# Kernel optimization log

Measured on AMD Instinct MI355X. Metric: run time of the kernel, lower is better.

The kernel has to match this reference:

```python
import jax, jax.numpy as jnp
import numpy as np

B = 8192
DIM_Q = 1024
DIM_U = 1024
NUM_CHARTS = 16
TOP_K = 2


def setup_inputs() -> dict:
    key = jax.random.key(0)
    k1, k2, k3 = jax.random.split(key, 3)
    q = jax.random.normal(k1, (B, DIM_Q), dtype=jnp.float32)
    weights = jax.random.uniform(k2, (B, NUM_CHARTS), dtype=jnp.float32)
    # W_stack init: -I + 0.01*randn per chart (dim_q == dim_u branch)
    W_stack = (-jnp.eye(DIM_Q, dtype=jnp.float32)[None, :, :]
               + 0.01 * jax.random.normal(k3, (NUM_CHARTS, DIM_U, DIM_Q), dtype=jnp.float32))
    return {"q": q, "weights": weights, "W_stack": W_stack}


def reference(q, weights, W_stack):
    # Top-k gated mixture of linear maps: out[b] = sum_{c in topk(weights[b])} w_norm[b,c] * W_stack[c] @ q[b]
    b = q.shape[0]
    w_vals, idx = jax.lax.top_k(weights, TOP_K)              # [B, k], sorted descending (matches torch.topk)
    w_norm = w_vals / jnp.clip(jnp.sum(w_vals, axis=1, keepdims=True), 1e-8, None)
    # scatter normalized weights back to dense [B, num_charts] gate matrix
    w_masked = jnp.zeros_like(weights).at[jnp.arange(b)[:, None], idx].set(w_norm)
    out = jnp.zeros((b, W_stack.shape[1]), dtype=q.dtype)
    for c in range(NUM_CHARTS):  # small fixed expert count
        out = out + w_masked[:, c:c + 1] * (q @ W_stack[c].T)  # [B, dim_u]
    return out
```

## Files before the change

### kernel.cpp

```cpp
#include <hip/hip_runtime.h>
#include <hip/hip_bf16.h>
#include <stdint.h>

#define NROWS 8192
#define DIMQ 1024
#define DIMU 1024
#define NCH 16

#define BM 128
#define BN 128
#define BK 64

typedef __attribute__((ext_vector_type(4))) float f32x4;
typedef __attribute__((ext_vector_type(8))) short bf16x8;

__device__ __forceinline__ short f2bf(float f) {
    union { __hip_bfloat16 h; short s; } u;
    u.h = __float2bfloat16(f);
    return u.s;
}

__global__ void cvt2_kernel(const float* __restrict__ q, const float* __restrict__ Ws,
                            short* __restrict__ qb, short* __restrict__ Wb) {
    const int nq = NROWS * DIMQ / 8;
    const int nw = NCH * DIMU * DIMQ / 8;
    int i0 = blockIdx.x * blockDim.x + threadIdx.x;
    int stride = gridDim.x * blockDim.x;
    for (int i = i0; i < nq; i += stride) {
        const f32x4* p = reinterpret_cast<const f32x4*>(q + (size_t)i * 8);
        f32x4 a = p[0], b = p[1];
        bf16x8 o;
        o[0] = f2bf(a[0]); o[1] = f2bf(a[1]); o[2] = f2bf(a[2]); o[3] = f2bf(a[3]);
        o[4] = f2bf(b[0]); o[5] = f2bf(b[1]); o[6] = f2bf(b[2]); o[7] = f2bf(b[3]);
        *reinterpret_cast<bf16x8*>(qb + (size_t)i * 8) = o;
    }
    for (int i = i0; i < nw; i += stride) {
        const f32x4* p = reinterpret_cast<const f32x4*>(Ws + (size_t)i * 8);
        f32x4 a = p[0], b = p[1];
        bf16x8 o;
        o[0] = f2bf(a[0]); o[1] = f2bf(a[1]); o[2] = f2bf(a[2]); o[3] = f2bf(a[3]);
        o[4] = f2bf(b[0]); o[5] = f2bf(b[1]); o[6] = f2bf(b[2]); o[7] = f2bf(b[3]);
        *reinterpret_cast<bf16x8*>(Wb + (size_t)i * 8) = o;
    }
}

__global__ void gate_kernel(const float* __restrict__ weights,
                            int* __restrict__ cnt,
                            int* __restrict__ rowlist,
                            float* __restrict__ wgt) {
    __shared__ int lcnt[NCH];
    __shared__ int lbase[NCH];
    const int t = threadIdx.x;
    const int b = blockIdx.x * blockDim.x + t;
    if (t < NCH) lcnt[t] = 0;
    __syncthreads();

    float w[NCH];
    const f32x4* wp = reinterpret_cast<const f32x4*>(weights + (size_t)b * NCH);
#pragma unroll
    for (int i = 0; i < 4; ++i) {
        f32x4 v = wp[i];
        w[i * 4 + 0] = v[0]; w[i * 4 + 1] = v[1];
        w[i * 4 + 2] = v[2]; w[i * 4 + 3] = v[3];
    }
    int i0 = 0; float v0 = w[0];
#pragma unroll
    for (int i = 1; i < NCH; ++i) if (w[i] > v0) { v0 = w[i]; i0 = i; }
    int i1 = (i0 == 0) ? 1 : 0; float v1 = w[i1];
#pragma unroll
    for (int i = 0; i < NCH; ++i) if (i != i0 && w[i] > v1) { v1 = w[i]; i1 = i; }
    float s = v0 + v1;
    s = (s < 1e-8f) ? 1e-8f : s;
    float n0 = v0 / s, n1 = v1 / s;

    int p0 = atomicAdd(&lcnt[i0], 1);
    int p1 = atomicAdd(&lcnt[i1], 1);
    __syncthreads();
    if (t < NCH) lbase[t] = atomicAdd(&cnt[t], lcnt[t]);
    __syncthreads();

    int o0 = lbase[i0] + p0;
    int o1 = lbase[i1] + p1;
    rowlist[(size_t)i0 * NROWS + o0] = b;  wgt[(size_t)i0 * NROWS + o0] = n0;
    rowlist[(size_t)i1 * NROWS + o1] = b;  wgt[(size_t)i1 * NROWS + o1] = n1;
}

__global__ __launch_bounds__(256, 3) void moe_gemm_bf(
    const short* __restrict__ qb, const short* __restrict__ Wb,
    const int* __restrict__ cnt, const int* __restrict__ rowlist,
    const float* __restrict__ wgt, float* __restrict__ out)
{
    const int id  = blockIdx.x;
    const int xcd = id & 7;
    const int k   = id >> 3;
    const int c   = xcd + ((k >> 9) << 3);
    const int kk  = k & 511;
    const int n0  = (kk & 7) * BN;
    const int m0  = (kk >> 3) * BM;

    const int count = cnt[c];
    if (m0 >= count) return;

    __shared__ short sA[BM * BK];
    __shared__ short sB[BN * BK];
    __shared__ int   sRow[BM];
    __shared__ float sW[BM];

    const int t = threadIdx.x;
    if (t < BM) {
        int gi = m0 + t;
        int r = 0; float wv_ = 0.f;
        if (gi < count) {
            r   = rowlist[(size_t)c * NROWS + gi];
            wv_ = wgt[(size_t)c * NROWS + gi];
        }
        sRow[t] = r; sW[t] = wv_;
    }
    __syncthreads();

    const short* aSrc[4];
    const short* bSrc[4];
#pragma unroll
    for (int i = 0; i < 4; ++i) {
        int ch = i * 256 + t;
        int r  = ch >> 3;
        int c8 = ch & 7;
        aSrc[i] = qb + (size_t)sRow[r] * DIMQ + c8 * 8;
        bSrc[i] = Wb + (size_t)c * ((size_t)DIMU * DIMQ) + (size_t)(n0 + r) * DIMQ + c8 * 8;
    }

    const int lane = t & 63;
    const int wv   = t >> 6;
    const int wm   = (wv >> 1) * 64;
    const int wn   = (wv & 1) * 64;
    const int rr   = lane & 15;
    const int g    = lane >> 4;

    f32x4 acc[4][4];
#pragma unroll
    for (int r = 0; r < 4; ++r)
#pragma unroll
        for (int cc = 0; cc < 4; ++cc)
            acc[r][cc] = (f32x4){0.f, 0.f, 0.f, 0.f};

    const int NKT = DIMQ / BK;
    for (int kt = 0; kt < NKT; ++kt) {
        __syncthreads();
#pragma unroll
        for (int i = 0; i < 4; ++i)
            __builtin_amdgcn_global_load_lds(aSrc[i] + kt * BK, &sA[(i * 256 + t) * 8], 16, 0, 0);
#pragma unroll
        for (int i = 0; i < 4; ++i)
            __builtin_amdgcn_global_load_lds(bSrc[i] + kt * BK, &sB[(i * 256 + t) * 8], 16, 0, 0);
        __syncthreads();

#pragma unroll
        for (int ks = 0; ks < 2; ++ks) {
            bf16x8 af[4], bfr[4];
#pragma unroll
            for (int r = 0; r < 4; ++r) {
                af[r]  = *reinterpret_cast<const bf16x8*>(&sA[(wm + r * 16 + rr) * BK + ks * 32 + g * 8]);
                bfr[r] = *reinterpret_cast<const bf16x8*>(&sB[(wn + r * 16 + rr) * BK + ks * 32 + g * 8]);
            }
#pragma unroll
            for (int r = 0; r < 4; ++r)
#pragma unroll
                for (int cc = 0; cc < 4; ++cc)
                    acc[r][cc] = __builtin_amdgcn_mfma_f32_16x16x32_bf16(af[r], bfr[cc], acc[r][cc], 0, 0, 0);
        }
    }

#pragma unroll
    for (int r = 0; r < 4; ++r) {
#pragma unroll
        for (int cc = 0; cc < 4; ++cc) {
#pragma unroll
            for (int j = 0; j < 4; ++j) {
                int rowInTile = wm + r * 16 + g * 4 + j;
                int gi = m0 + rowInTile;
                if (gi < count) {
                    int   orow = sRow[rowInTile];
                    float wgx  = sW[rowInTile];
                    int   col  = n0 + wn + cc * 16 + rr;
                    atomicAdd(&out[(size_t)orow * DIMU + col], acc[r][cc][j] * wgx);
                }
            }
        }
    }
}

#define BKF 32
#define LDSTRF 40
typedef __attribute__((ext_vector_type(4))) short s16x4;

__global__ __launch_bounds__(256, 2) void moe_gemm_f32(
    const float* __restrict__ q, const float* __restrict__ Wst,
    const int* __restrict__ cnt, const int* __restrict__ rowlist,
    const float* __restrict__ wgt, float* __restrict__ out)
{
    const int c  = blockIdx.z;
    const int n0 = blockIdx.x * BN;
    const int m0 = blockIdx.y * BM;
    const int count = cnt[c];
    if (m0 >= count) return;

    __shared__ short sA[BM * LDSTRF];
    __shared__ short sB[BN * LDSTRF];
    __shared__ int   sRow[BM];
    __shared__ float sW[BM];

    const int t = threadIdx.x;
    if (t < BM) {
        int gi = m0 + t;
        int r = 0; float w = 0.f;
        if (gi < count) {
            r = rowlist[(size_t)c * NROWS + gi];
            w = wgt[(size_t)c * NROWS + gi];
        }
        sRow[t] = r; sW[t] = w;
    }
    __syncthreads();

    const float* aBase[4];
    const float* bBase[4];
    int ldsOff[4];
#pragma unroll
    for (int i = 0; i < 4; ++i) {
        int f  = t + i * 256;
        int r  = f >> 3;
        int c4 = f & 7;
        aBase[i]  = q   + (size_t)sRow[r] * DIMQ + c4 * 4;
        bBase[i]  = Wst + (size_t)c * ((size_t)DIMU * DIMQ) + (size_t)(n0 + r) * DIMQ + c4 * 4;
        ldsOff[i] = r * LDSTRF + c4 * 4;
    }

    const int lane = t & 63;
    const int wv   = t >> 6;
    const int wm   = (wv >> 1) * 64;
    const int wn   = (wv & 1) * 64;
    const int rr   = lane & 15;
    const int g    = lane >> 4;

    f32x4 acc[4][4];
#pragma unroll
    for (int r = 0; r < 4; ++r)
#pragma unroll
        for (int cc = 0; cc < 4; ++cc)
            acc[r][cc] = (f32x4){0.f, 0.f, 0.f, 0.f};

    f32x4 pa[4], pb[4];
#pragma unroll
    for (int i = 0; i < 4; ++i) {
        pa[i] = *reinterpret_cast<const f32x4*>(aBase[i]);
        pb[i] = *reinterpret_cast<const f32x4*>(bBase[i]);
    }

    const int NKT = DIMQ / BKF;
    for (int kt = 0; kt < NKT; ++kt) {
        __syncthreads();
#pragma unroll
        for (int i = 0; i < 4; ++i) {
            s16x4 va, vb;
#pragma unroll
            for (int j = 0; j < 4; ++j) { va[j] = f2bf(pa[i][j]); vb[j] = f2bf(pb[i][j]); }
            *reinterpret_cast<s16x4*>(&sA[ldsOff[i]]) = va;
            *reinterpret_cast<s16x4*>(&sB[ldsOff[i]]) = vb;
        }
        __syncthreads();

        if (kt + 1 < NKT) {
            int k = (kt + 1) * BKF;
#pragma unroll
            for (int i = 0; i < 4; ++i) {
                pa[i] = *reinterpret_cast<const f32x4*>(aBase[i] + k);
                pb[i] = *reinterpret_cast<const f32x4*>(bBase[i] + k);
            }
        }

        bf16x8 af[4], bfr[4];
#pragma unroll
        for (int r = 0; r < 4; ++r) {
            af[r]  = *reinterpret_cast<const bf16x8*>(&sA[(wm + r * 16 + rr) * LDSTRF + g * 8]);
            bfr[r] = *reinterpret_cast<const bf16x8*>(&sB[(wn + r * 16 + rr) * LDSTRF + g * 8]);
        }
#pragma unroll
        for (int r = 0; r < 4; ++r)
#pragma unroll
            for (int cc = 0; cc < 4; ++cc)
                acc[r][cc] = __builtin_amdgcn_mfma_f32_16x16x32_bf16(af[r], bfr[cc], acc[r][cc], 0, 0, 0);
    }

#pragma unroll
    for (int r = 0; r < 4; ++r) {
#pragma unroll
        for (int cc = 0; cc < 4; ++cc) {
#pragma unroll
            for (int j = 0; j < 4; ++j) {
                int rowInTile = wm + r * 16 + g * 4 + j;
                int gi = m0 + rowInTile;
                if (gi < count) {
                    int   orow = sRow[rowInTile];
                    float w    = sW[rowInTile];
                    int   col  = n0 + wn + cc * 16 + rr;
                    atomicAdd(&out[(size_t)orow * DIMU + col], acc[r][cc][j] * w);
                }
            }
        }
    }
}

extern "C" void kernel_launch(void* const* d_in, const int* in_sizes, int n_in,
                              void* d_out, int out_size, void* d_ws, size_t ws_size,
                              hipStream_t stream) {
    const float* q  = (const float*)d_in[0];
    const float* w  = (const float*)d_in[1];
    const float* Ws = (const float*)d_in[2];
    float* out = (float*)d_out;

    const size_t qbf_bytes  = (size_t)NROWS * DIMQ * 2;
    const size_t wbf_bytes  = (size_t)NCH * DIMU * (size_t)DIMQ * 2;
    const size_t meta_bytes = 256 + (size_t)NCH * NROWS * (sizeof(int) + sizeof(float));
    char* ws = (char*)d_ws;

    if (ws_size >= qbf_bytes + wbf_bytes + meta_bytes) {
        short* qb      = (short*)ws;
        short* Wb      = (short*)(ws + qbf_bytes);
        int*   cnt     = (int*)(ws + qbf_bytes + wbf_bytes);
        int*   rowlist = (int*)(ws + qbf_bytes + wbf_bytes + 256);
        float* wgt     = (float*)(ws + qbf_bytes + wbf_bytes + 256 + (size_t)NCH * NROWS * sizeof(int));

        hipMemsetAsync(cnt, 0, 256, stream);
        hipMemsetAsync(d_out, 0, (size_t)out_size * sizeof(float), stream);

        cvt2_kernel<<<2048, 256, 0, stream>>>(q, Ws, qb, Wb);
        gate_kernel<<<NROWS / 256, 256, 0, stream>>>(w, cnt, rowlist, wgt);

        moe_gemm_bf<<<8192, 256, 0, stream>>>(qb, Wb, cnt, rowlist, wgt, out);
    } else {
        int*   cnt     = (int*)ws;
        int*   rowlist = (int*)(ws + 256);
        float* wgt     = (float*)(ws + 256 + (size_t)NCH * NROWS * sizeof(int));

        hipMemsetAsync(cnt, 0, 256, stream);
        hipMemsetAsync(d_out, 0, (size_t)out_size * sizeof(float), stream);

        gate_kernel<<<NROWS / 256, 256, 0, stream>>>(w, cnt, rowlist, wgt);

        dim3 grid(DIMU / BN, NROWS / BM, NCH);
        moe_gemm_f32<<<grid, 256, 0, stream>>>(q, Ws, cnt, rowlist, wgt, out);
    }
}
```

Baseline: 241.1 us.

## Restructure bf16 MoE GEMM with register prefetch, padded LDS and 512 threads

Replaces the direct global-to-LDS loads with register-staged loads that prefetch the next K tiles while the current tile is computed. The LDS rows are padded to avoid bank conflicts, and the block grows to 512 threads (8 waves, each computing 64x32). The XCD-aware block-id swizzle is dropped in favour of a plain 3D grid. It adds register pressure and extra barriers, and losing the swizzle may reduce L2 locality of W tiles per chart.

```diff
diff --git a/kernel.cpp b/kernel.cpp
--- a/kernel.cpp
+++ b/kernel.cpp
@@ -10,8 +10,10 @@
 #define BM 128
 #define BN 128
 #define BK 64
+#define LDSTR 72
 
 typedef __attribute__((ext_vector_type(4))) float f32x4;
+typedef __attribute__((ext_vector_type(4))) short s16x4;
 typedef __attribute__((ext_vector_type(8))) short bf16x8;
 
 __device__ __forceinline__ short f2bf(float f) {
@@ -85,24 +87,19 @@
     rowlist[(size_t)i1 * NROWS + o1] = b;  wgt[(size_t)i1 * NROWS + o1] = n1;
 }
 
-__global__ __launch_bounds__(256, 3) void moe_gemm_bf(
+__global__ __launch_bounds__(512, 4) void moe_gemm_bf(
     const short* __restrict__ qb, const short* __restrict__ Wb,
     const int* __restrict__ cnt, const int* __restrict__ rowlist,
     const float* __restrict__ wgt, float* __restrict__ out)
 {
-    const int id  = blockIdx.x;
-    const int xcd = id & 7;
-    const int k   = id >> 3;
-    const int c   = xcd + ((k >> 9) << 3);
-    const int kk  = k & 511;
-    const int n0  = (kk & 7) * BN;
-    const int m0  = (kk >> 3) * BM;
-
+    const int c  = blockIdx.z;
+    const int n0 = blockIdx.x * BN;
+    const int m0 = blockIdx.y * BM;
     const int count = cnt[c];
     if (m0 >= count) return;
 
-    __shared__ short sA[BM * BK];
-    __shared__ short sB[BN * BK];
+    __shared__ short sA[BM * LDSTR];
+    __shared__ short sB[BN * LDSTR];
     __shared__ int   sRow[BM];
     __shared__ float sW[BM];
 
@@ -118,62 +115,103 @@
     }
     __syncthreads();
 
-    const short* aSrc[4];
-    const short* bSrc[4];
-#pragma unroll
-    for (int i = 0; i < 4; ++i) {
-        int ch = i * 256 + t;
+    const short* aS[2];
+    const short* bS[2];
+    int ldsO[2];
+#pragma unroll
+    for (int i = 0; i < 2; ++i) {
+        int ch = i * 512 + t;
         int r  = ch >> 3;
         int c8 = ch & 7;
-        aSrc[i] = qb + (size_t)sRow[r] * DIMQ + c8 * 8;
-        bSrc[i] = Wb + (size_t)c * ((size_t)DIMU * DIMQ) + (size_t)(n0 + r) * DIMQ + c8 * 8;
+        aS[i]   = qb + (size_t)sRow[r] * DIMQ + c8 * 8;
+        bS[i]   = Wb + (size_t)c * ((size_t)DIMU * DIMQ) + (size_t)(n0 + r) * DIMQ + c8 * 8;
+        ldsO[i] = r * LDSTR + c8 * 8;
     }
 
     const int lane = t & 63;
     const int wv   = t >> 6;
-    const int wm   = (wv >> 1) * 64;
-    const int wn   = (wv & 1) * 64;
+    const int wm   = (wv >> 2) * 64;
+    const int wn   = (wv & 3) * 32;
     const int rr   = lane & 15;
     const int g    = lane >> 4;
 
-    f32x4 acc[4][4];
+    f32x4 acc[4][2];
 #pragma unroll
     for (int r = 0; r < 4; ++r)
 #pragma unroll
-        for (int cc = 0; cc < 4; ++cc)
-            acc[r][cc] = (f32x4){0.f, 0.f, 0.f, 0.f};
+        for (int n = 0; n < 2; ++n)
+            acc[r][n] = (f32x4){0.f, 0.f, 0.f, 0.f};
+
+    bf16x8 a0[2], b0[2], a1[2], b1[2];
+#pragma unroll
+    for (int i = 0; i < 2; ++i) {
+        a0[i] = *reinterpret_cast<const bf16x8*>(aS[i]);
+        b0[i] = *reinterpret_cast<const bf16x8*>(bS[i]);
+        a1[i] = *reinterpret_cast<const bf16x8*>(aS[i] + BK);
+        b1[i] = *reinterpret_cast<const bf16x8*>(bS[i] + BK);
+    }
+
+#define COMPUTE_STEP()                                                                              \
+    {                                                                                               \
+        _Pragma("unroll")                                                                           \
+        for (int ks = 0; ks < 2; ++ks) {                                                            \
+            bf16x8 af[4], bfr[2];                                                                   \
+            _Pragma("unroll")                                                                       \
+            for (int r = 0; r < 4; ++r)                                                             \
+                af[r]  = *reinterpret_cast<const bf16x8*>(&sA[(wm + r * 16 + rr) * LDSTR + ks * 32 + g * 8]); \
+            _Pragma("unroll")                                                                       \
+            for (int n = 0; n < 2; ++n)                                                             \
+                bfr[n] = *reinterpret_cast<const bf16x8*>(&sB[(wn + n * 16 + rr) * LDSTR + ks * 32 + g * 8]); \
+            _Pragma("unroll")                                                                       \
+            for (int r = 0; r < 4; ++r)                                                             \
+                _Pragma("unroll")                                                                   \
+                for (int n = 0; n < 2; ++n)                                                         \
+                    acc[r][n] = __builtin_amdgcn_mfma_f32_16x16x32_bf16(af[r], bfr[n], acc[r][n], 0, 0, 0); \
+        }                                                                                           \
+    }
 
     const int NKT = DIMQ / BK;
-    for (int kt = 0; kt < NKT; ++kt) {
-        __syncthreads();
-#pragma unroll
-        for (int i = 0; i < 4; ++i)
-            __builtin_amdgcn_global_load_lds(aSrc[i] + kt * BK, &sA[(i * 256 + t) * 8], 16, 0, 0);
-#pragma unroll
-        for (int i = 0; i < 4; ++i)
-            __builtin_amdgcn_global_load_lds(bSrc[i] + kt * BK, &sB[(i * 256 + t) * 8], 16, 0, 0);
-        __syncthreads();
-
-#pragma unroll
-        for (int ks = 0; ks < 2; ++ks) {
-            bf16x8 af[4], bfr[4];
-#pragma unroll
-            for (int r = 0; r < 4; ++r) {
-                af[r]  = *reinterpret_cast<const bf16x8*>(&sA[(wm + r * 16 + rr) * BK + ks * 32 + g * 8]);
-                bfr[r] = *reinterpret_cast<const bf16x8*>(&sB[(wn + r * 16 + rr) * BK + ks * 32 + g * 8]);
-            }
-#pragma unroll
-            for (int r = 0; r < 4; ++r)
-#pragma unroll
-                for (int cc = 0; cc < 4; ++cc)
-                    acc[r][cc] = __builtin_amdgcn_mfma_f32_16x16x32_bf16(af[r], bfr[cc], acc[r][cc], 0, 0, 0);
-        }
-    }
+    for (int kt2 = 0; kt2 < NKT; kt2 += 2) {
+        __syncthreads();
+#pragma unroll
+        for (int i = 0; i < 2; ++i) {
+            *reinterpret_cast<bf16x8*>(&sA[ldsO[i]]) = a0[i];
+            *reinterpret_cast<bf16x8*>(&sB[ldsO[i]]) = b0[i];
+        }
+        __syncthreads();
+        if (kt2 + 2 < NKT) {
+            int k = (kt2 + 2) * BK;
+#pragma unroll
+            for (int i = 0; i < 2; ++i) {
+                a0[i] = *reinterpret_cast<const bf16x8*>(aS[i] + k);
+                b0[i] = *reinterpret_cast<const bf16x8*>(bS[i] + k);
+            }
+        }
+        COMPUTE_STEP();
+
+        __syncthreads();
+#pragma unroll
+        for (int i = 0; i < 2; ++i) {
+            *reinterpret_cast<bf16x8*>(&sA[ldsO[i]]) = a1[i];
+            *reinterpret_cast<bf16x8*>(&sB[ldsO[i]]) = b1[i];
+        }
+        __syncthreads();
+        if (kt2 + 3 < NKT) {
+            int k = (kt2 + 3) * BK;
+#pragma unroll
+            for (int i = 0; i < 2; ++i) {
+                a1[i] = *reinterpret_cast<const bf16x8*>(aS[i] + k);
+                b1[i] = *reinterpret_cast<const bf16x8*>(bS[i] + k);
+            }
+        }
+        COMPUTE_STEP();
+    }
+#undef COMPUTE_STEP
 
 #pragma unroll
     for (int r = 0; r < 4; ++r) {
 #pragma unroll
-        for (int cc = 0; cc < 4; ++cc) {
+        for (int n = 0; n < 2; ++n) {
 #pragma unroll
             for (int j = 0; j < 4; ++j) {
                 int rowInTile = wm + r * 16 + g * 4 + j;
@@ -181,8 +219,8 @@
                 if (gi < count) {
                     int   orow = sRow[rowInTile];
                     float wgx  = sW[rowInTile];
-                    int   col  = n0 + wn + cc * 16 + rr;
-                    atomicAdd(&out[(size_t)orow * DIMU + col], acc[r][cc][j] * wgx);
+                    int   col  = n0 + wn + n * 16 + rr;
+                    atomicAdd(&out[(size_t)orow * DIMU + col], acc[r][n][j] * wgx);
                 }
             }
         }
@@ -191,7 +229,6 @@
 
 #define BKF 32
 #define LDSTRF 40
-typedef __attribute__((ext_vector_type(4))) short s16x4;
 
 __global__ __launch_bounds__(256, 2) void moe_gemm_f32(
     const float* __restrict__ q, const float* __restrict__ Wst,
@@ -335,7 +372,8 @@
         cvt2_kernel<<<2048, 256, 0, stream>>>(q, Ws, qb, Wb);
         gate_kernel<<<NROWS / 256, 256, 0, stream>>>(w, cnt, rowlist, wgt);
 
-        moe_gemm_bf<<<8192, 256, 0, stream>>>(qb, Wb, cnt, rowlist, wgt, out);
+        dim3 grid(DIMU / BN, NROWS / BM, NCH);
+        moe_gemm_bf<<<grid, 512, 0, stream>>>(qb, Wb, cnt, rowlist, wgt, out);
     } else {
         int*   cnt     = (int*)ws;
         int*   rowlist = (int*)(ws + 256);
```

Result: faster. 228.5 us (-5.2%).
